# Kernel tuning notes

Measured on AMD Instinct MI355X. Metric: run time of the kernel, lower is better.

## Reference

```python
import jax, jax.numpy as jnp
import numpy as np

PI = 3.1415926
MAX_V = 8  # max vertices of a quad-quad convex intersection
ALPHA, GAMMA, IOU_THRES = 0.25, 2.0, 0.5


def xyxy2xywh_a(b):
    cx = (b[..., 0] + b[..., 2]) * 0.5
    cy = (b[..., 1] + b[..., 3]) * 0.5
    w = b[..., 2] - b[..., 0]
    h = b[..., 3] - b[..., 1]
    return jnp.stack([cx, cy, w, h, b[..., 4]], -1)


def rbox_2_quad(b):
    # [N,5] (x1,y1,x2,y2,theta_deg) -> [N,4,2] corner quads
    x = xyxy2xywh_a(b)
    cx, cy, w, h, t = x[:, 0], x[:, 1], x[:, 2], x[:, 3], x[:, 4]
    th = t * (PI / 180.0)
    c, s = jnp.cos(th), jnp.sin(th)
    dx = jnp.array([-0.5, 0.5, 0.5, -0.5], b.dtype)
    dy = jnp.array([-0.5, -0.5, 0.5, 0.5], b.dtype)
    px = cx[:, None] + dx * w[:, None] * c[:, None] - dy * h[:, None] * s[:, None]
    py = cy[:, None] + dx * w[:, None] * s[:, None] + dy * h[:, None] * c[:, None]
    return jnp.stack([px, py], -1)


def min_area_square(b):
    cx = (b[:, 0] + b[:, 2]) * 0.5
    cy = (b[:, 1] + b[:, 3]) * 0.5
    s = jnp.maximum(b[:, 2] - b[:, 0], b[:, 3] - b[:, 1]) * 0.5
    return jnp.stack([cx - s, cy - s, cx + s, cy + s], 1)


def bbox_overlaps(a, b):
    # axis-aligned IoU matrix [N,M]
    lt = jnp.maximum(a[:, None, :2], b[None, :, :2])
    rb = jnp.minimum(a[:, None, 2:], b[None, :, 2:])
    wh = jnp.clip(rb - lt, 0.0)
    inter = wh[..., 0] * wh[..., 1]
    area_a = (a[:, 2] - a[:, 0]) * (a[:, 3] - a[:, 1])
    area_b = (b[:, 2] - b[:, 0]) * (b[:, 3] - b[:, 1])
    return inter / (area_a[:, None] + area_b[None, :] - inter + 1e-6)


def points_in_quads(pts, quads):
    # pointsJf: pts [A,2] inside convex quads [G,4,2] -> [A,G] {0,1}
    e = jnp.roll(quads, -1, axis=1) - quads  # [G,4,2]
    rel = pts[:, None, None, :] - quads[None]  # [A,G,4,2]
    cr = e[None, ..., 0] * rel[..., 1] - e[None, ..., 1] * rel[..., 0]
    inside = jnp.all(cr >= 0, -1) | jnp.all(cr <= 0, -1)
    return inside.astype(pts.dtype)


def _signed_area2(q):
    return jnp.sum(q[:, 0] * jnp.roll(q[:, 1], -1) - jnp.roll(q[:, 0], -1) * q[:, 1])


def _quad_inter_area(q1, q2):
    # Sutherland-Hodgman clipping of quad q1 by convex quad q2, fixed 8-vertex buffer
    q1 = jnp.where(_signed_area2(q1) < 0, q1[::-1], q1)
    q2 = jnp.where(_signed_area2(q2) < 0, q2[::-1], q2)
    poly = jnp.zeros((MAX_V, 2), q1.dtype).at[:4].set(q1)
    edges = jnp.stack([q2, jnp.roll(q2, -1, axis=0)], 1)  # [4,2,2]

    def clip(carry, edge):
        poly, n = carry
        a, b = edge[0], edge[1]
        idx = jnp.arange(MAX_V)
        nidx = jnp.where(idx + 1 < n, idx + 1, 0)
        cur, nxt = poly, poly[nidx]
        d = b - a
        dc = d[0] * (cur[:, 1] - a[1]) - d[1] * (cur[:, 0] - a[0])
        dn = d[0] * (nxt[:, 1] - a[1]) - d[1] * (nxt[:, 0] - a[0])
        denom = dc - dn
        t = dc / jnp.where(jnp.abs(denom) < 1e-12, 1e-12, denom)
        inter = cur + t[:, None] * (nxt - cur)
        active = idx < n
        keep_cur = active & (dc >= 0)
        keep_int = active & ((dc >= 0) != (dn >= 0))
        pts = jnp.stack([cur, inter], 1).reshape(2 * MAX_V, 2)
        flags = jnp.stack([keep_cur, keep_int], 1).reshape(-1)
        pos = jnp.where(flags, jnp.cumsum(flags) - 1, MAX_V)
        newpoly = jnp.zeros((MAX_V + 1, 2), poly.dtype).at[pos].set(pts)[:MAX_V]
        return (newpoly, flags.sum()), None

    (poly, n), _ = jax.lax.scan(clip, (poly, jnp.int32(4)), edges)
    idx = jnp.arange(MAX_V)
    nidx = jnp.where(idx + 1 < n, idx + 1, 0)
    contrib = poly[:, 0] * poly[nidx, 1] - poly[nidx, 0] * poly[:, 1]
    area = 0.5 * jnp.abs(jnp.sum(jnp.where(idx < n, contrib, 0.0)))
    return jnp.where(n >= 3, area, 0.0)


def rbox_overlaps(quads_a, quads_g, gate, thresh=0.1):
    area_a = 0.5 * jnp.abs(jax.vmap(_signed_area2)(quads_a))
    area_g = 0.5 * jnp.abs(jax.vmap(_signed_area2)(quads_g))
    inter = jax.vmap(lambda qa: jax.vmap(lambda qg: _quad_inter_area(qa, qg))(quads_g))(quads_a)
    iou = inter / (area_a[:, None] + area_g[None, :] - inter + 1e-6)
    return jnp.where(gate > thresh, iou, 0.0)


def encode(anchors, gt):
    a = xyxy2xywh_a(anchors)
    g = xyxy2xywh_a(gt)
    dx = (g[:, 0] - a[:, 0]) / a[:, 2]
    dy = (g[:, 1] - a[:, 1]) / a[:, 3]
    dw = jnp.log(g[:, 2] / a[:, 2])
    dh = jnp.log(g[:, 3] / a[:, 3])
    dt = (g[:, 4] - a[:, 4]) * (PI / 180.0)
    return jnp.stack([dx, dy, dw, dh, dt], 1)


def decode(anchors, deltas):
    a = xyxy2xywh_a(anchors)
    cx = a[..., 0] + deltas[..., 0] * a[..., 2]
    cy = a[..., 1] + deltas[..., 1] * a[..., 3]
    w = a[..., 2] * jnp.exp(deltas[..., 2])
    h = a[..., 3] * jnp.exp(deltas[..., 3])
    t = a[..., 4] + deltas[..., 4] * (180.0 / PI)
    return jnp.stack([cx, cy, w, h, t], -1)


def smooth_l1(x, t, beta=1.0 / 9):
    diff = jnp.abs(x - t)
    return jnp.where(diff < beta, 0.5 * diff * diff / beta, diff - 0.5 * beta)


def _forward(classifications, regressions, anchors, annotations):
    B = classifications.shape[0]
    _ = decode(anchors, regressions)  # all_pred_boxes (unused when func='smooth')
    cls_losses, reg_losses = [], []
    for j in range(B):
        cls = jnp.clip(classifications[j], 1e-4, 1.0 - 1e-4)
        anch = anchors[j]
        gtb = annotations[j, :, :5]
        labels = annotations[j, :, 5].astype(jnp.int32)
        indicator = bbox_overlaps(min_area_square(anch), min_area_square(gtb))
        centers = xyxy2xywh_a(anch)[:, :2]
        quads_g = rbox_2_quad(gtb)
        inside = points_in_quads(centers, quads_g)
        quads_a = rbox_2_quad(anch)
        ious = rbox_overlaps(quads_a, quads_g, inside * indicator)  # [A,G]
        iou_max = ious.max(1)
        iou_argmax = ious.argmax(1)
        pos = iou_max >= IOU_THRES
        max_gt = ious.max(0)
        argmax_gt = ious.argmax(0)
        low = (max_gt < IOU_THRES).astype(jnp.int32)
        pos = (pos.astype(jnp.int32).at[argmax_gt].max(low)).astype(bool)
        num_pos = pos.sum()
        C = cls.shape[1]
        onehot = jax.nn.one_hot(labels[iou_argmax], C, dtype=cls.dtype)
        tgt = -jnp.ones_like(cls)
        tgt = jnp.where((iou_max < IOU_THRES - 0.1)[:, None], 0.0, tgt)
        tgt = jnp.where(pos[:, None], onehot, tgt)
        af = jnp.where(tgt == 1.0, ALPHA, 1.0 - ALPHA)
        fw = af * jnp.where(tgt == 1.0, 1.0 - cls, cls) ** GAMMA
        bce = -(tgt * jnp.log(cls + 1e-6) + (1.0 - tgt) * jnp.log(1.0 - cls + 1e-6))
        cls_loss = jnp.where(tgt != -1.0, fw * bce, 0.0).sum() / jnp.maximum(num_pos.astype(cls.dtype), 1.0)
        cls_losses.append(cls_loss)
        reg_t = encode(anch, gtb[iou_argmax])
        l = smooth_l1(regressions[j], reg_t)
        denom = (jnp.maximum(num_pos, 1) * l.shape[1]).astype(l.dtype)
        reg_loss = jnp.where(num_pos > 0, (l * pos[:, None].astype(l.dtype)).sum() / denom, 0.0)
        reg_losses.append(reg_loss)
    loss_cls = 5.0 * jnp.stack(cls_losses).mean(keepdims=True)
    loss_reg = 2.0 * jnp.stack(reg_losses).mean(keepdims=True)
    return loss_cls, loss_reg


def setup_inputs() -> dict:
    key = jax.random.key(0)
    ks = jax.random.split(key, 8)
    B, A, G, C = 2, 32768, 32, 15
    cls = jax.random.uniform(ks[0], (B, A, C), jnp.float32)
    reg = jax.random.normal(ks[1], (B, A, 5), jnp.float32) * 0.1
    ac = jax.random.uniform(ks[2], (B, A, 2), jnp.float32, 0.0, 1024.0)
    awh = jax.random.uniform(ks[3], (B, A, 2), jnp.float32, 16.0, 256.0)
    anchors = jnp.concatenate([ac - awh * 0.5, ac + awh * 0.5, jnp.zeros((B, A, 1), jnp.float32)], -1)
    gc = jax.random.uniform(ks[4], (B, G, 2), jnp.float32, 64.0, 960.0)
    gwh = jax.random.uniform(ks[5], (B, G, 2), jnp.float32, 24.0, 300.0)
    gt = jax.random.uniform(ks[6], (B, G, 1), jnp.float32, -90.0, 90.0)
    glab = jax.random.randint(ks[7], (B, G, 1), 0, C).astype(jnp.float32)
    annotations = jnp.concatenate([gc - gwh * 0.5, gc + gwh * 0.5, gt, glab], -1)
    return {"classifications": cls, "regressions": reg, "anchors": anchors, "annotations": annotations}


def reference(classifications, regressions, anchors, annotations):
    return _forward(classifications, regressions, anchors, annotations)
```

## Files before the change

### kernel.cpp

```cpp
#include <hip/hip_runtime.h>

#define A_N 32768
#define G_N 32
#define C_N 15
#define BPB 128
#define DEG2RAD ((float)(3.1415926 / 180.0))
#define BETA (1.0f / 9.0f)

typedef unsigned long long ull;

template <int NIN>
__device__ __forceinline__ int clip_pass(float ax, float ay, float dx, float dy,
                                         float (&PX)[8], float (&PY)[8], int n) {
  constexpr int NOUT = (NIN + 1 < 8) ? NIN + 1 : 8;
  float d[NIN];
#pragma unroll
  for (int i = 0; i < NIN; ++i)
    d[i] = dx * (PY[i] - ay) - dy * (PX[i] - ax);
  float NX[NOUT], NY[NOUT];
#pragma unroll
  for (int i = 0; i < NOUT; ++i) { NX[i] = 0.f; NY[i] = 0.f; }
  int m = 0;
#pragma unroll
  for (int i = 0; i < NIN; ++i) {
    if (i < n) {
      bool w = (i + 1 < n);
      float dn = w ? d[(i + 1) % NIN] : d[0];
      float xn = w ? PX[(i + 1) % NIN] : PX[0];
      float yn = w ? PY[(i + 1) % NIN] : PY[0];
      bool kc = (d[i] >= 0.f);
      bool kn = (dn >= 0.f);
      if (kc) {
#pragma unroll
        for (int o = 0; o < NOUT; ++o)
          if (o <= 2 * i && m == o) { NX[o] = PX[i]; NY[o] = PY[i]; }
        ++m;
      }
      if (kc != kn) {
        float den = d[i] - dn;
        if (fabsf(den) < 1e-12f) den = 1e-12f;
        float t = d[i] / den;
        float ix = PX[i] + t * (xn - PX[i]);
        float iy = PY[i] + t * (yn - PY[i]);
#pragma unroll
        for (int o = 0; o < NOUT; ++o)
          if (o <= 2 * i + 1 && m == o) { NX[o] = ix; NY[o] = iy; }
        ++m;
      }
    }
  }
#pragma unroll
  for (int i = 0; i < NOUT; ++i) { PX[i] = NX[i]; PY[i] = NY[i]; }
#pragma unroll
  for (int i = NOUT; i < 8; ++i) { PX[i] = 0.f; PY[i] = 0.f; }
  return m;
}

__global__ void k_init(ull* gbest, int B) {
  int t = threadIdx.x;
  if (t < B * G_N) gbest[t] = 0xFFFFFFFFull;
}

__global__ __launch_bounds__(256) void k_main(
    const float* __restrict__ anchors, const float* __restrict__ annot,
    float* __restrict__ iou_max, int* __restrict__ iou_arg,
    int* __restrict__ posf, ull* __restrict__ gbest) {
  int j = blockIdx.x >> 7;
  int blk = blockIdx.x & (BPB - 1);
  int tid = threadIdx.x;
  int a = blk * 256 + tid;

  __shared__ float g_qx[G_N][4], g_qy[G_N][4];
  __shared__ float g_sq[G_N][4];
  __shared__ float g_sarea[G_N], g_qarea[G_N];
  __shared__ float a_q[256][8];
  __shared__ float a_area[256];
  __shared__ ull rowbest[256];
  __shared__ ull colmax[G_N];
  __shared__ unsigned short list[256 * G_N];
  __shared__ int cnt;

  if (tid == 0) cnt = 0;
  rowbest[tid] = 0xFFFFFFFFull;
  if (tid < G_N) colmax[tid] = 0xFFFFFFFFull;

  if (tid < G_N) {
    const float* g = annot + ((size_t)j * G_N + tid) * 6;
    float x1 = g[0], y1 = g[1], x2 = g[2], y2 = g[3], t = g[4];
    float cxx = (x1 + x2) * 0.5f, cyy = (y1 + y2) * 0.5f;
    float w = x2 - x1, h = y2 - y1;
    float th = t * DEG2RAD;
    float c = cosf(th), s = sinf(th);
    const float ddx[4] = {-0.5f, 0.5f, 0.5f, -0.5f};
    const float ddy[4] = {-0.5f, -0.5f, 0.5f, 0.5f};
    float px[4], py[4];
#pragma unroll
    for (int k = 0; k < 4; ++k) {
      px[k] = cxx + ddx[k] * w * c - ddy[k] * h * s;
      py[k] = cyy + ddx[k] * w * s + ddy[k] * h * c;
    }
    float s2 = 0.f;
#pragma unroll
    for (int k = 0; k < 4; ++k)
      s2 += px[k] * py[(k + 1) & 3] - px[(k + 1) & 3] * py[k];
    if (s2 < 0.f) {
#pragma unroll
      for (int k = 0; k < 4; ++k) { g_qx[tid][k] = px[3 - k]; g_qy[tid][k] = py[3 - k]; }
    } else {
#pragma unroll
      for (int k = 0; k < 4; ++k) { g_qx[tid][k] = px[k]; g_qy[tid][k] = py[k]; }
    }
    g_qarea[tid] = 0.5f * fabsf(s2);
    float half = fmaxf(w, h) * 0.5f;
    float sx1 = cxx - half, sy1 = cyy - half, sx2 = cxx + half, sy2 = cyy + half;
    g_sq[tid][0] = sx1; g_sq[tid][1] = sy1; g_sq[tid][2] = sx2; g_sq[tid][3] = sy2;
    g_sarea[tid] = (sx2 - sx1) * (sy2 - sy1);
  }

  const float* an = anchors + ((size_t)j * A_N + a) * 5;
  float ax1 = an[0], ay1 = an[1], ax2 = an[2], ay2 = an[3], at = an[4];
  float acx = (ax1 + ax2) * 0.5f, acy = (ay1 + ay2) * 0.5f;
  float aw = ax2 - ax1, ah = ay2 - ay1;
  float ath = at * DEG2RAD;
  float ac = cosf(ath), asn = sinf(ath);
  {
    const float ddx[4] = {-0.5f, 0.5f, 0.5f, -0.5f};
    const float ddy[4] = {-0.5f, -0.5f, 0.5f, 0.5f};
    float apx[4], apy[4];
#pragma unroll
    for (int k = 0; k < 4; ++k) {
      apx[k] = acx + ddx[k] * aw * ac - ddy[k] * ah * asn;
      apy[k] = acy + ddx[k] * aw * asn + ddy[k] * ah * ac;
    }
    float s2a = 0.f;
#pragma unroll
    for (int k = 0; k < 4; ++k)
      s2a += apx[k] * apy[(k + 1) & 3] - apx[(k + 1) & 3] * apy[k];
    if (s2a < 0.f) {
      float tx = apx[0], ty = apy[0];
      apx[0] = apx[3]; apy[0] = apy[3]; apx[3] = tx; apy[3] = ty;
      tx = apx[1]; ty = apy[1];
      apx[1] = apx[2]; apy[1] = apy[2]; apx[2] = tx; apy[2] = ty;
    }
#pragma unroll
    for (int k = 0; k < 4; ++k) { a_q[tid][k] = apx[k]; a_q[tid][4 + k] = apy[k]; }
    a_area[tid] = 0.5f * fabsf(s2a);
  }
  float half = fmaxf(aw, ah) * 0.5f;
  float asx1 = acx - half, asy1 = acy - half, asx2 = acx + half, asy2 = acy + half;
  float asarea = (asx2 - asx1) * (asy2 - asy1);
  __syncthreads();

  for (int g = 0; g < G_N; ++g) {
    float ltx = fmaxf(asx1, g_sq[g][0]);
    float lty = fmaxf(asy1, g_sq[g][1]);
    float rbx = fminf(asx2, g_sq[g][2]);
    float rby = fminf(asy2, g_sq[g][3]);
    float iw = fmaxf(rbx - ltx, 0.f);
    float ih = fmaxf(rby - lty, 0.f);
    float inter_s = iw * ih;
    float ind = inter_s / (asarea + g_sarea[g] - inter_s + 1e-6f);
    bool pall = true, nall = true;
#pragma unroll
    for (int k = 0; k < 4; ++k) {
      float ex = g_qx[g][(k + 1) & 3] - g_qx[g][k];
      float ey = g_qy[g][(k + 1) & 3] - g_qy[g][k];
      float rx = acx - g_qx[g][k];
      float ry = acy - g_qy[g][k];
      float cr = ex * ry - ey * rx;
      pall = pall && (cr >= 0.f);
      nall = nall && (cr <= 0.f);
    }
    if ((pall || nall) && ind > 0.1f) {
      int p = atomicAdd(&cnt, 1);
      list[p] = (unsigned short)((tid << 5) | g);
    }
  }
  __syncthreads();

  int np = cnt;
  for (int i = tid; i < np; i += 256) {
    int ent = list[i];
    int la = ent >> 5, g = ent & 31;
    float PX[8], PY[8];
#pragma unroll
    for (int k = 0; k < 4; ++k) { PX[k] = a_q[la][k]; PY[k] = a_q[la][4 + k]; }
#pragma unroll
    for (int k = 4; k < 8; ++k) { PX[k] = 0.f; PY[k] = 0.f; }
    float gx0 = g_qx[g][0], gy0 = g_qy[g][0];
    float gx1 = g_qx[g][1], gy1 = g_qy[g][1];
    float gx2 = g_qx[g][2], gy2 = g_qy[g][2];
    float gx3 = g_qx[g][3], gy3 = g_qy[g][3];
    int n = 4;
    n = clip_pass<4>(gx0, gy0, gx1 - gx0, gy1 - gy0, PX, PY, n);
    n = clip_pass<5>(gx1, gy1, gx2 - gx1, gy2 - gy1, PX, PY, n);
    n = clip_pass<6>(gx2, gy2, gx3 - gx2, gy3 - gy2, PX, PY, n);
    n = clip_pass<7>(gx3, gy3, gx0 - gx3, gy0 - gy3, PX, PY, n);
    float s = 0.f;
#pragma unroll
    for (int k = 0; k < 8; ++k) {
      if (k < n) {
        float xn = (k + 1 < n) ? PX[(k + 1) & 7] : PX[0];
        float yn = (k + 1 < n) ? PY[(k + 1) & 7] : PY[0];
        s += PX[k] * yn - xn * PY[k];
      }
    }
    float inter = (n >= 3) ? 0.5f * fabsf(s) : 0.f;
    float v = inter / (a_area[la] + g_qarea[g] - inter + 1e-6f);
    ull pr = ((ull)__float_as_uint(v) << 32) | (unsigned)(~(unsigned)g);
    atomicMax(&rowbest[la], pr);
    unsigned ga = (unsigned)(blk * 256 + la);
    ull pc = ((ull)__float_as_uint(v) << 32) | (unsigned)(~ga);
    atomicMax(&colmax[g], pc);
  }
  __syncthreads();

  size_t ia = (size_t)j * A_N + a;
  ull rb = rowbest[tid];
  float best = __uint_as_float((unsigned)(rb >> 32));
  int barg = (int)(~(unsigned)rb);
  iou_max[ia] = best;
  iou_arg[ia] = barg;
  posf[ia] = (best >= 0.5f) ? 1 : 0;
  if (tid < G_N) atomicMax(&gbest[(size_t)j * G_N + tid], colmax[tid]);
}

__global__ __launch_bounds__(256) void k_loss(
    const float* __restrict__ cls_in, const float* __restrict__ reg_in,
    const float* __restrict__ anchors, const float* __restrict__ annot,
    const float* __restrict__ iou_max, const int* __restrict__ iou_arg,
    const int* __restrict__ posf, const ull* __restrict__ gbest,
    float* __restrict__ cls_part, float* __restrict__ reg_part,
    int* __restrict__ cnt_part) {
  int j = blockIdx.x >> 7;
  int blk = blockIdx.x & (BPB - 1);
  int tid = threadIdx.x;
  int a = blk * 256 + tid;

  __shared__ int lab[G_N];
  __shared__ float gcx[G_N], gcy[G_N], gw[G_N], gh[G_N], gth[G_N];
  __shared__ int forced[G_N];
  if (tid < G_N) {
    const float* g = annot + ((size_t)j * G_N + tid) * 6;
    gcx[tid] = (g[0] + g[2]) * 0.5f;
    gcy[tid] = (g[1] + g[3]) * 0.5f;
    gw[tid] = g[2] - g[0];
    gh[tid] = g[3] - g[1];
    gth[tid] = g[4];
    lab[tid] = (int)g[5];
    ull p = gbest[(size_t)j * G_N + tid];
    float v = __uint_as_float((unsigned)(p >> 32));
    forced[tid] = (v < 0.5f) ? (int)(~(unsigned)p) : -1;
  }
  __syncthreads();

  size_t ia = (size_t)j * A_N + a;
  float im = iou_max[ia];
  int arg = iou_arg[ia];
  int p = posf[ia];
#pragma unroll
  for (int g2 = 0; g2 < G_N; ++g2)
    if (forced[g2] == a) p = 1;
  int lb = lab[arg];
  const float* c = cls_in + ia * C_N;

  float csum = 0.f;
  bool bg = (im < 0.4f);
#pragma unroll
  for (int ci = 0; ci < C_N; ++ci) {
    float pc = fminf(fmaxf(c[ci], 1e-4f), 0.9999f);
    int tgt;
    if (p) tgt = (ci == lb) ? 1 : 0;
    else if (bg) tgt = 0;
    else continue;
    if (tgt == 1)
      csum += 0.25f * (1.f - pc) * (1.f - pc) * (-logf(pc + 1e-6f));
    else
      csum += 0.75f * pc * pc * (-logf(1.f - pc + 1e-6f));
  }

  float rsum = 0.f;
  if (p) {
    const float* an = anchors + ia * 5;
    float ax1 = an[0], ay1 = an[1], ax2 = an[2], ay2 = an[3], at = an[4];
    float acx = (ax1 + ax2) * 0.5f, acy = (ay1 + ay2) * 0.5f;
    float aw = ax2 - ax1, ah = ay2 - ay1;
    const float* r = reg_in + ia * 5;
    float t5[5];
    t5[0] = (gcx[arg] - acx) / aw;
    t5[1] = (gcy[arg] - acy) / ah;
    t5[2] = logf(gw[arg] / aw);
    t5[3] = logf(gh[arg] / ah);
    t5[4] = (gth[arg] - at) * DEG2RAD;
#pragma unroll
    for (int i = 0; i < 5; ++i) {
      float d = fabsf(r[i] - t5[i]);
      rsum += (d < BETA) ? (0.5f * d * d / BETA) : (d - 0.5f * BETA);
    }
  }

  __shared__ float s1[256], s2[256];
  __shared__ int s3[256];
  s1[tid] = csum; s2[tid] = rsum; s3[tid] = p;
  __syncthreads();
  for (int o = 128; o; o >>= 1) {
    if (tid < o) { s1[tid] += s1[tid + o]; s2[tid] += s2[tid + o]; s3[tid] += s3[tid + o]; }
    __syncthreads();
  }
  if (tid == 0) {
    cls_part[blockIdx.x] = s1[0];
    reg_part[blockIdx.x] = s2[0];
    cnt_part[blockIdx.x] = s3[0];
  }
}

__global__ void k_final(const float* cls_part, const float* reg_part,
                        const int* cnt_part, float* out, int B) {
  if (threadIdx.x == 0 && blockIdx.x == 0) {
    float cl = 0.f, rl = 0.f;
    for (int j = 0; j < B; ++j) {
      float cs = 0.f, rs = 0.f;
      int np = 0;
      for (int b = 0; b < BPB; ++b) {
        cs += cls_part[j * BPB + b];
        rs += reg_part[j * BPB + b];
        np += cnt_part[j * BPB + b];
      }
      float npf = (np > 0) ? (float)np : 1.f;
      cl += cs / npf;
      rl += (np > 0) ? rs / (npf * 5.f) : 0.f;
    }
    out[0] = 5.0f * cl / (float)B;
    out[1] = 2.0f * rl / (float)B;
  }
}

extern "C" void kernel_launch(void* const* d_in, const int* in_sizes, int n_in,
                              void* d_out, int out_size, void* d_ws, size_t ws_size,
                              hipStream_t stream) {
  const float* cls = (const float*)d_in[0];
  const float* reg = (const float*)d_in[1];
  const float* anc = (const float*)d_in[2];
  const float* ann = (const float*)d_in[3];
  int B = in_sizes[3] / (G_N * 6);

  char* w = (char*)d_ws;
  ull* gbest = (ull*)w;        w += (size_t)B * G_N * sizeof(ull);
  float* iou_max = (float*)w;  w += (size_t)B * A_N * 4;
  int* iou_arg = (int*)w;      w += (size_t)B * A_N * 4;
  int* posf = (int*)w;         w += (size_t)B * A_N * 4;
  float* cls_part = (float*)w; w += (size_t)B * BPB * 4;
  float* reg_part = (float*)w; w += (size_t)B * BPB * 4;
  int* cnt_part = (int*)w;     w += (size_t)B * BPB * 4;

  k_init<<<1, 64, 0, stream>>>(gbest, B);
  k_main<<<B * BPB, 256, 0, stream>>>(anc, ann, iou_max, iou_arg, posf, gbest);
  k_loss<<<B * BPB, 256, 0, stream>>>(cls, reg, anc, ann, iou_max, iou_arg, posf,
                                      gbest, cls_part, reg_part, cnt_part);
  k_final<<<1, 1, 0, stream>>>(cls_part, reg_part, cnt_part, (float*)d_out, B);
}
```

Baseline: 42.43 us.

## Remove init and final kernels via per-block partials and last-block reduction

Drops the init kernel by writing per-block column maxima to a partial buffer, which each loss block then reduces itself instead of relying on global atomicMax. The final single-thread kernel is folded into the loss kernel using a done counter, so the last block to finish computes the output. It also preloads class scores, merges the target branches and switches to fast __logf. This cuts two kernel launches and the serial tail, at the cost of redundant gpart reads in every loss block and slightly lower log precision.

```diff
diff --git a/kernel.cpp b/kernel.cpp
--- a/kernel.cpp
+++ b/kernel.cpp
@@ -56,19 +56,17 @@
   return m;
 }
 
-__global__ void k_init(ull* gbest, int B) {
-  int t = threadIdx.x;
-  if (t < B * G_N) gbest[t] = 0xFFFFFFFFull;
-}
-
 __global__ __launch_bounds__(256) void k_main(
     const float* __restrict__ anchors, const float* __restrict__ annot,
     float* __restrict__ iou_max, int* __restrict__ iou_arg,
-    int* __restrict__ posf, ull* __restrict__ gbest) {
+    int* __restrict__ posf, ull* __restrict__ gpart, unsigned* done) {
   int j = blockIdx.x >> 7;
   int blk = blockIdx.x & (BPB - 1);
   int tid = threadIdx.x;
   int a = blk * 256 + tid;
+
+  if (blockIdx.x == 0 && tid == 0)
+    __hip_atomic_store(done, 0u, __ATOMIC_RELAXED, __HIP_MEMORY_SCOPE_AGENT);
 
   __shared__ float g_qx[G_N][4], g_qy[G_N][4];
   __shared__ float g_sq[G_N][4];
@@ -222,24 +220,39 @@
   iou_max[ia] = best;
   iou_arg[ia] = barg;
   posf[ia] = (best >= 0.5f) ? 1 : 0;
-  if (tid < G_N) atomicMax(&gbest[(size_t)j * G_N + tid], colmax[tid]);
+  if (tid < G_N)
+    gpart[((size_t)j * BPB + blk) * G_N + tid] = colmax[tid];
 }
 
 __global__ __launch_bounds__(256) void k_loss(
     const float* __restrict__ cls_in, const float* __restrict__ reg_in,
     const float* __restrict__ anchors, const float* __restrict__ annot,
     const float* __restrict__ iou_max, const int* __restrict__ iou_arg,
-    const int* __restrict__ posf, const ull* __restrict__ gbest,
+    const int* __restrict__ posf, const ull* __restrict__ gpart,
     float* __restrict__ cls_part, float* __restrict__ reg_part,
-    int* __restrict__ cnt_part) {
+    int* __restrict__ cnt_part, unsigned* done, float* __restrict__ out, int B) {
   int j = blockIdx.x >> 7;
   int blk = blockIdx.x & (BPB - 1);
   int tid = threadIdx.x;
   int a = blk * 256 + tid;
+  (void)blk;
 
   __shared__ int lab[G_N];
   __shared__ float gcx[G_N], gcy[G_N], gw[G_N], gh[G_N], gth[G_N];
+  __shared__ ull sred[8][G_N];
   __shared__ int forced[G_N];
+
+  {
+    int g = tid & 31, chunk = tid >> 5;
+    const ull* gp = gpart + (size_t)j * BPB * G_N;
+    ull m = 0;
+#pragma unroll
+    for (int b = 0; b < BPB / 8; ++b) {
+      ull v = gp[(size_t)(chunk * (BPB / 8) + b) * G_N + g];
+      m = v > m ? v : m;
+    }
+    sred[chunk][g] = m;
+  }
   if (tid < G_N) {
     const float* g = annot + ((size_t)j * G_N + tid) * 6;
     gcx[tid] = (g[0] + g[2]) * 0.5f;
@@ -248,9 +261,14 @@
     gh[tid] = g[3] - g[1];
     gth[tid] = g[4];
     lab[tid] = (int)g[5];
-    ull p = gbest[(size_t)j * G_N + tid];
-    float v = __uint_as_float((unsigned)(p >> 32));
-    forced[tid] = (v < 0.5f) ? (int)(~(unsigned)p) : -1;
+  }
+  __syncthreads();
+  if (tid < G_N) {
+    ull m = sred[0][tid];
+#pragma unroll
+    for (int c = 1; c < 8; ++c) m = sred[c][tid] > m ? sred[c][tid] : m;
+    float v = __uint_as_float((unsigned)(m >> 32));
+    forced[tid] = (v < 0.5f) ? (int)(~(unsigned)m) : -1;
   }
   __syncthreads();
 
@@ -264,19 +282,22 @@
   int lb = lab[arg];
   const float* c = cls_in + ia * C_N;
 
+  float pcv[C_N];
+#pragma unroll
+  for (int ci = 0; ci < C_N; ++ci) pcv[ci] = c[ci];
+
   float csum = 0.f;
   bool bg = (im < 0.4f);
-#pragma unroll
-  for (int ci = 0; ci < C_N; ++ci) {
-    float pc = fminf(fmaxf(c[ci], 1e-4f), 0.9999f);
-    int tgt;
-    if (p) tgt = (ci == lb) ? 1 : 0;
-    else if (bg) tgt = 0;
-    else continue;
-    if (tgt == 1)
-      csum += 0.25f * (1.f - pc) * (1.f - pc) * (-logf(pc + 1e-6f));
-    else
-      csum += 0.75f * pc * pc * (-logf(1.f - pc + 1e-6f));
+  if (p || bg) {
+#pragma unroll
+    for (int ci = 0; ci < C_N; ++ci) {
+      float pc = fminf(fmaxf(pcv[ci], 1e-4f), 0.9999f);
+      bool tgt1 = p && (ci == lb);
+      if (tgt1)
+        csum += 0.25f * (1.f - pc) * (1.f - pc) * (-__logf(pc + 1e-6f));
+      else
+        csum += 0.75f * pc * pc * (-__logf(1.f - pc + 1e-6f));
+    }
   }
 
   float rsum = 0.f;
@@ -289,8 +310,8 @@
     float t5[5];
     t5[0] = (gcx[arg] - acx) / aw;
     t5[1] = (gcy[arg] - acy) / ah;
-    t5[2] = logf(gw[arg] / aw);
-    t5[3] = logf(gh[arg] / ah);
+    t5[2] = __logf(gw[arg] / aw);
+    t5[3] = __logf(gh[arg] / ah);
     t5[4] = (gth[arg] - at) * DEG2RAD;
 #pragma unroll
     for (int i = 0; i < 5; ++i) {
@@ -307,31 +328,48 @@
     if (tid < o) { s1[tid] += s1[tid + o]; s2[tid] += s2[tid + o]; s3[tid] += s3[tid + o]; }
     __syncthreads();
   }
+
+  __shared__ int amLast;
   if (tid == 0) {
-    cls_part[blockIdx.x] = s1[0];
-    reg_part[blockIdx.x] = s2[0];
-    cnt_part[blockIdx.x] = s3[0];
-  }
-}
-
-__global__ void k_final(const float* cls_part, const float* reg_part,
-                        const int* cnt_part, float* out, int B) {
-  if (threadIdx.x == 0 && blockIdx.x == 0) {
-    float cl = 0.f, rl = 0.f;
-    for (int j = 0; j < B; ++j) {
-      float cs = 0.f, rs = 0.f;
-      int np = 0;
-      for (int b = 0; b < BPB; ++b) {
-        cs += cls_part[j * BPB + b];
-        rs += reg_part[j * BPB + b];
-        np += cnt_part[j * BPB + b];
-      }
-      float npf = (np > 0) ? (float)np : 1.f;
-      cl += cs / npf;
-      rl += (np > 0) ? rs / (npf * 5.f) : 0.f;
-    }
-    out[0] = 5.0f * cl / (float)B;
-    out[1] = 2.0f * rl / (float)B;
+    __hip_atomic_store(&cls_part[blockIdx.x], s1[0], __ATOMIC_RELAXED, __HIP_MEMORY_SCOPE_AGENT);
+    __hip_atomic_store(&reg_part[blockIdx.x], s2[0], __ATOMIC_RELAXED, __HIP_MEMORY_SCOPE_AGENT);
+    __hip_atomic_store(&cnt_part[blockIdx.x], s3[0], __ATOMIC_RELAXED, __HIP_MEMORY_SCOPE_AGENT);
+    __threadfence();
+    unsigned old = __hip_atomic_fetch_add(done, 1u, __ATOMIC_ACQ_REL, __HIP_MEMORY_SCOPE_AGENT);
+    amLast = (old == (unsigned)(gridDim.x - 1)) ? 1 : 0;
+  }
+  __syncthreads();
+
+  if (amLast) {
+    int P = (int)gridDim.x;
+    float cv = 0.f, rv = 0.f;
+    int nv = 0;
+    if (tid < P) {
+      cv = __hip_atomic_load(&cls_part[tid], __ATOMIC_RELAXED, __HIP_MEMORY_SCOPE_AGENT);
+      rv = __hip_atomic_load(&reg_part[tid], __ATOMIC_RELAXED, __HIP_MEMORY_SCOPE_AGENT);
+      nv = __hip_atomic_load(&cnt_part[tid], __ATOMIC_RELAXED, __HIP_MEMORY_SCOPE_AGENT);
+    }
+    __syncthreads();
+    s1[tid] = cv; s2[tid] = rv; s3[tid] = nv;
+    __syncthreads();
+    for (int o = 64; o; o >>= 1) {
+      if ((tid & 127) < o) {
+        s1[tid] += s1[tid + o]; s2[tid] += s2[tid + o]; s3[tid] += s3[tid + o];
+      }
+      __syncthreads();
+    }
+    if (tid == 0) {
+      float cl = 0.f, rl = 0.f;
+      for (int jj = 0; jj < B; ++jj) {
+        float cs = s1[jj * 128], rs = s2[jj * 128];
+        int np = s3[jj * 128];
+        float npf = (np > 0) ? (float)np : 1.f;
+        cl += cs / npf;
+        rl += (np > 0) ? rs / (npf * 5.f) : 0.f;
+      }
+      out[0] = 5.0f * cl / (float)B;
+      out[1] = 2.0f * rl / (float)B;
+    }
   }
 }
 
@@ -345,17 +383,17 @@
   int B = in_sizes[3] / (G_N * 6);
 
   char* w = (char*)d_ws;
-  ull* gbest = (ull*)w;        w += (size_t)B * G_N * sizeof(ull);
-  float* iou_max = (float*)w;  w += (size_t)B * A_N * 4;
-  int* iou_arg = (int*)w;      w += (size_t)B * A_N * 4;
-  int* posf = (int*)w;         w += (size_t)B * A_N * 4;
-  float* cls_part = (float*)w; w += (size_t)B * BPB * 4;
-  float* reg_part = (float*)w; w += (size_t)B * BPB * 4;
-  int* cnt_part = (int*)w;     w += (size_t)B * BPB * 4;
-
-  k_init<<<1, 64, 0, stream>>>(gbest, B);
-  k_main<<<B * BPB, 256, 0, stream>>>(anc, ann, iou_max, iou_arg, posf, gbest);
+  unsigned* done = (unsigned*)w;  w += 64;
+  ull* gpart = (ull*)w;           w += (size_t)B * BPB * G_N * sizeof(ull);
+  float* iou_max = (float*)w;     w += (size_t)B * A_N * 4;
+  int* iou_arg = (int*)w;         w += (size_t)B * A_N * 4;
+  int* posf = (int*)w;            w += (size_t)B * A_N * 4;
+  float* cls_part = (float*)w;    w += (size_t)B * BPB * 4;
+  float* reg_part = (float*)w;    w += (size_t)B * BPB * 4;
+  int* cnt_part = (int*)w;        w += (size_t)B * BPB * 4;
+
+  k_main<<<B * BPB, 256, 0, stream>>>(anc, ann, iou_max, iou_arg, posf, gpart, done);
   k_loss<<<B * BPB, 256, 0, stream>>>(cls, reg, anc, ann, iou_max, iou_arg, posf,
-                                      gbest, cls_part, reg_part, cnt_part);
-  k_final<<<1, 1, 0, stream>>>(cls_part, reg_part, cnt_part, (float*)d_out, B);
+                                      gpart, cls_part, reg_part, cnt_part, done,
+                                      (float*)d_out, B);
 }
```

Result: faster. 37.36 us (-12.0%).
